# Kernel tuning notes

Hardware: AMD Instinct MI355X
Metric: run time of the kernel (lower is better)

Reference implementation:

```python
import jax, jax.numpy as jnp
import numpy as np

D = 32          # embedding_size
B = 16384       # batch_size
P = 16          # neighbor_sample_size (paths per item per hop)
NE = 100000     # n_entity
NU = 100000     # n_user
NR = 32         # n_relation
N_ITER = 2


def setup_inputs() -> dict:
    key = jax.random.key(0)
    ks = jax.random.split(key, 20)
    s = 0.1
    nrm = lambda k, sh: jax.random.normal(k, sh, dtype=jnp.float32) * s
    inp = {
        "user_table": nrm(ks[0], (NU, D)),
        "ent_table": nrm(ks[1], (NE, D)),
        "rel_table": nrm(ks[2], (NR, D)),
        # PyTorch LSTM params, gate order (i, f, g, o)
        "w_ih0": nrm(ks[3], (4 * D, 2 * D)),
        "w_hh0": nrm(ks[4], (4 * D, D)),
        "b_ih0": nrm(ks[5], (4 * D,)),
        "b_hh0": nrm(ks[6], (4 * D,)),
        "w_ih1": nrm(ks[7], (4 * D, 2 * D)),
        "w_hh1": nrm(ks[8], (4 * D, D)),
        "b_ih1": nrm(ks[9], (4 * D,)),
        "b_hh1": nrm(ks[10], (4 * D,)),
        "agg_w": nrm(ks[11], (D, D)),
        "agg_b": nrm(ks[12], (D,)),
        "users": jax.random.randint(ks[13], (B,), 0, NU),
        "items": jax.random.randint(ks[14], (B,), 0, NE),
        "ratings": jax.random.randint(ks[15], (B,), 0, 2),
        # hop h path table: [n_entity, P, 2*(h+1)+1]; values < 32 valid for both tables
        "lp0": jax.random.randint(ks[16], (NE, P, 3), 0, 32),
        "lp1": jax.random.randint(ks[17], (NE, P, 5), 0, 32),
    }
    return inp


def _lstm_last(seq, w_ih, w_hh, b_ih, b_hh):
    # seq: [N, T, 2D] -> final hidden state [N, D], PyTorch gate order i,f,g,o
    N = seq.shape[0]
    H = w_hh.shape[1]
    bias = b_ih + b_hh

    def step(carry, x):
        h, c = carry
        g = x @ w_ih.T + h @ w_hh.T + bias
        i, f, gg, o = jnp.split(g, 4, axis=-1)
        c = jax.nn.sigmoid(f) * c + jax.nn.sigmoid(i) * jnp.tanh(gg)
        h = jax.nn.sigmoid(o) * jnp.tanh(c)
        return (h, c), None

    h0 = jnp.zeros((N, H), seq.dtype)
    (h, _), _ = jax.lax.scan(step, (h0, h0), jnp.swapaxes(seq, 0, 1))
    return h


def _forward(user_table, ent_table, rel_table, lstm_params, agg_w, agg_b,
             users, items, ratings, lps):
    u = user_table[users]                # [B, D]
    items_emb = ent_table[items]         # [B, D]
    for hop in range(N_ITER):
        lp = lps[hop]
        w_ih, w_hh, b_ih, b_hh = lstm_params[hop]
        il = lp[items]                   # [B, P, 2*(hop+1)+1]
        seed_e = ent_table[il[:, :, 0]]  # [B, P, D]
        u_b = jnp.broadcast_to(u[:, None, :], seed_e.shape)
        first = jnp.concatenate([u_b, seed_e], -1)[:, :, None, :]   # [B,P,1,2D]
        rel_e = rel_table[il[:, :, 1::2]]                            # [B,P,hop+1,D]
        tail_e = ent_table[il[:, :, 2::2]]                           # [B,P,hop+1,D]
        rest = jnp.concatenate([rel_e, tail_e], -1)                  # [B,P,hop+1,2D]
        seq = jnp.concatenate([first, rest], 2).reshape(B * P, hop + 2, 2 * D)
        h = _lstm_last(seq, w_ih, w_hh, b_ih, b_hh)                  # [B*P, D]
        final = h.reshape(B, P, D).sum(axis=1)                       # hidden_out sum
        items_emb = (items_emb + final) @ agg_w.T + agg_b            # 'sum' aggregator
    scores = jnp.sum(u * items_emb, axis=-1)                         # [B]
    r = ratings.astype(scores.dtype)
    # stable BCE on sigmoid(scores)
    loss = -jnp.mean(r * jax.nn.log_sigmoid(scores) + (1.0 - r) * jax.nn.log_sigmoid(-scores))
    return loss, jax.nn.sigmoid(scores)


def reference(user_table, ent_table, rel_table,
              w_ih0, w_hh0, b_ih0, b_hh0,
              w_ih1, w_hh1, b_ih1, b_hh1,
              agg_w, agg_b,
              users, items, ratings, lp0, lp1):
    lstm_params = [(w_ih0, w_hh0, b_ih0, b_hh0), (w_ih1, w_hh1, b_ih1, b_hh1)]
    loss, scores_normalized = _forward(user_table, ent_table, rel_table,
                                       lstm_params, agg_w, agg_b,
                                       users, items, ratings, (lp0, lp1))
    return (loss, scores_normalized, items)
```

## Files before the change

### kernel.cpp

```cpp
#include <hip/hip_runtime.h>
#include <math.h>

#define D  32
#define BN 16384
#define PP 16

typedef __bf16 bf16x8 __attribute__((ext_vector_type(8)));
typedef float  floatx4 __attribute__((ext_vector_type(4)));

#define IMG_BYTES   29184
#define WIH_OFF     0
#define WHH_OFF     18432
#define BIAS_OFF    28672
#define X_OFF       29184
#define H_OFF       38400
#define LDS_BYTES   43520

__device__ __forceinline__ float sigf(float x) {
    float e = __builtin_amdgcn_exp2f(-x * 1.44269504088896341f);
    return __builtin_amdgcn_rcpf(1.0f + e);
}
__device__ __forceinline__ float tanh_fast(float x) {
    float e = __builtin_amdgcn_exp2f(x * 2.88539008177792681f);
    return 1.0f - 2.0f * __builtin_amdgcn_rcpf(e + 1.0f);
}
__device__ __forceinline__ float logsigf(float x) {
    float ax = fabsf(x);
    float l = log1pf(__expf(-ax));
    return (x >= 0.0f) ? -l : x - l;
}

__device__ __forceinline__ void stage16(const float* __restrict__ src, char* dst) {
    const float4* s = (const float4*)src;
    float4 a = s[0], b = s[1], c = s[2], d = s[3];
    bf16x8 lo = { (__bf16)a.x, (__bf16)a.y, (__bf16)a.z, (__bf16)a.w,
                  (__bf16)b.x, (__bf16)b.y, (__bf16)b.z, (__bf16)b.w };
    bf16x8 hi = { (__bf16)c.x, (__bf16)c.y, (__bf16)c.z, (__bf16)c.w,
                  (__bf16)d.x, (__bf16)d.y, (__bf16)d.z, (__bf16)d.w };
    *(bf16x8*)dst        = lo;
    *(bf16x8*)(dst + 16) = hi;
}

__global__ __launch_bounds__(256)
void prep_weights(const float* __restrict__ w_ih, const float* __restrict__ w_hh,
                  const float* __restrict__ b_ih, const float* __restrict__ b_hh,
                  float* __restrict__ img_f)
{
    char* base = (char*)img_f;
    const int t0 = blockIdx.x * 256 + threadIdx.x;
    for (int idx = t0; idx < 8192; idx += 2048) {
        int n = idx >> 6, k = idx & 63;
        ((__bf16*)(base + WIH_OFF))[n * 72 + k] = (__bf16)w_ih[idx];
    }
    for (int idx = t0; idx < 4096; idx += 2048) {
        int n = idx >> 5, k = idx & 31;
        ((__bf16*)(base + WHH_OFF))[n * 40 + k] = (__bf16)w_hh[idx];
    }
    if (t0 < 128)
        ((float*)(base + BIAS_OFF))[t0] = b_ih[t0] + b_hh[t0];
}

template<int L, int T>
__global__ __launch_bounds__(256, 2)
void hop_mfma(const float* __restrict__ user_table,
              const float* __restrict__ ent_table,
              const float* __restrict__ rel_table,
              const float* __restrict__ img,
              const int*   __restrict__ users,
              const int*   __restrict__ items,
              const int*   __restrict__ lp,
              float* __restrict__ final_out)
{
    __shared__ __align__(16) char lds[LDS_BYTES];

    const int tid  = threadIdx.x;
    const int lane = tid & 63;
    const int wave = tid >> 6;

    {
        const float4* g = (const float4*)img;
        float4* l = (float4*)lds;
        #pragma unroll
        for (int i = 0; i < 8; ++i) {
            int idx = i * 256 + tid;
            if (idx < IMG_BYTES / 16) l[idx] = g[idx];
        }
    }
    __syncthreads();

    char* Wih  = lds + WIH_OFF;
    char* Whh  = lds + WHH_OFF;
    const float* bias = (const float*)(lds + BIAS_OFF);
    char* Xl   = lds + X_OFF;
    char* Hl   = lds + H_OFF;

    const int srow  = tid >> 2;
    const int squad = tid & 3;
    const int spair = blockIdx.x * 64 + srow;
    const int sb    = spair >> 4;
    const int sp    = spair & 15;
    const int sitem = items[sb];
    const int suser = users[sb];
    const int* __restrict__ sil = lp + ((size_t)sitem * PP + sp) * L;
    char* sdst = Xl + srow * 144 + squad * 32;

    const int wrow = wave * 16;
    const int am   = wrow + (lane & 15);
    const int ak   = (lane >> 4) * 8;
    const int bnl  = lane & 15;

    float cst[8]  = {0,0,0,0,0,0,0,0};
    float hout[8];
    floatx4 acc[8];
    #pragma unroll
    for (int nt = 0; nt < 8; ++nt) {
        float bv = bias[nt * 16 + bnl];
        floatx4 v = { bv, bv, bv, bv };
        acc[nt] = v;
    }

    #pragma unroll
    for (int t = 0; t < T; ++t) {
        {
            const float* src;
            if (t == 0) {
                src = (squad < 2) ? user_table + (size_t)suser * D + squad * 16
                                  : ent_table + (size_t)sil[0] * D + (squad - 2) * 16;
            } else {
                src = (squad < 2) ? rel_table + (size_t)sil[2 * t - 1] * D + squad * 16
                                  : ent_table + (size_t)sil[2 * t]     * D + (squad - 2) * 16;
            }
            stage16(src, sdst);
        }

        bf16x8 ax0 = *(const bf16x8*)(Xl + am * 144 + ak * 2);
        bf16x8 ax1 = *(const bf16x8*)(Xl + am * 144 + 64 + ak * 2);
        bf16x8 ah  = {};
        if (t > 0) ah = *(const bf16x8*)(Hl + am * 80 + ak * 2);

        #pragma unroll
        for (int nt = 0; nt < 8; ++nt) {
            const int bn = nt * 16 + bnl;
            bf16x8 b0 = *(const bf16x8*)(Wih + bn * 144 + ak * 2);
            bf16x8 b1 = *(const bf16x8*)(Wih + bn * 144 + 64 + ak * 2);
            floatx4 a = acc[nt];
            a = __builtin_amdgcn_mfma_f32_16x16x32_bf16(ax0, b0, a, 0, 0, 0);
            a = __builtin_amdgcn_mfma_f32_16x16x32_bf16(ax1, b1, a, 0, 0, 0);
            if (t > 0) {
                bf16x8 bh = *(const bf16x8*)(Whh + bn * 80 + ak * 2);
                a = __builtin_amdgcn_mfma_f32_16x16x32_bf16(ah, bh, a, 0, 0, 0);
            }
            acc[nt] = a;
        }

        #pragma unroll
        for (int ng = 0; ng < 2; ++ng) {
            floatx4 gi = acc[ng], gf = acc[ng + 2], gg = acc[ng + 4], go = acc[ng + 6];
            #pragma unroll
            for (int r = 0; r < 4; ++r) {
                float c = cst[ng * 4 + r];
                c = sigf(gf[r]) * c + sigf(gi[r]) * tanh_fast(gg[r]);
                cst[ng * 4 + r] = c;
                float h = sigf(go[r]) * tanh_fast(c);
                hout[ng * 4 + r] = h;
                if (t < T - 1) {
                    int pr = wrow + (lane >> 4) * 4 + r;
                    int un = ng * 16 + bnl;
                    *(__bf16*)(Hl + pr * 80 + un * 2) = (__bf16)h;
                }
            }
        }

        if (t < T - 1) {
            #pragma unroll
            for (int nt = 0; nt < 8; ++nt) {
                float bv = bias[nt * 16 + bnl];
                floatx4 v = { bv, bv, bv, bv };
                acc[nt] = v;
            }
        }
    }

    const int fb = blockIdx.x * 4 + wave;
    #pragma unroll
    for (int ng = 0; ng < 2; ++ng) {
        float v = hout[ng * 4 + 0] + hout[ng * 4 + 1] + hout[ng * 4 + 2] + hout[ng * 4 + 3];
        v += __shfl_xor(v, 16);
        v += __shfl_xor(v, 32);
        if (lane < 16)
            final_out[(size_t)fb * D + ng * 16 + lane] = v;
    }
}

__global__ __launch_bounds__(256)
void agg_kernel(const float* __restrict__ src_emb,
                const float* __restrict__ ent_table,
                const int*   __restrict__ items,
                const float* __restrict__ final_in,
                const float* __restrict__ agg_w,
                const float* __restrict__ agg_b,
                float* __restrict__ out_emb)
{
    const int t = blockIdx.x * 256 + threadIdx.x;
    const int b = t >> 5;
    const int j = t & 31;
    const float* __restrict__ src =
        src_emb ? (src_emb + (size_t)b * D) : (ent_table + (size_t)items[b] * D);
    const float* __restrict__ fin = final_in + (size_t)b * D;
    const float* __restrict__ w   = agg_w + (size_t)j * D;
    float acc = agg_b[j];
    #pragma unroll
    for (int k = 0; k < D; ++k) acc = fmaf(src[k] + fin[k], w[k], acc);
    out_emb[t] = acc;
}

__global__ __launch_bounds__(256)
void score_kernel(const float* __restrict__ user_table,
                  const float* __restrict__ emb,
                  const int*   __restrict__ users,
                  const int*   __restrict__ items,
                  const int*   __restrict__ ratings,
                  float* __restrict__ out,
                  float* __restrict__ partials)
{
    __shared__ float red[4];
    const int t = threadIdx.x;
    const int b = blockIdx.x * 256 + t;
    const float* __restrict__ u = user_table + (size_t)users[b] * D;
    const float* __restrict__ e = emb + (size_t)b * D;
    float s = 0.0f;
    #pragma unroll
    for (int k = 0; k < D; ++k) s = fmaf(u[k], e[k], s);
    out[1 + b]      = sigf(s);
    out[1 + BN + b] = (float)items[b];
    float r = (float)ratings[b];
    float term = r * logsigf(s) + (1.0f - r) * logsigf(-s);
    #pragma unroll
    for (int m = 1; m < 64; m <<= 1) term += __shfl_xor(term, m);
    if ((t & 63) == 0) red[t >> 6] = term;
    __syncthreads();
    if (t == 0) partials[blockIdx.x] = red[0] + red[1] + red[2] + red[3];
}

__global__ void loss_kernel(const float* __restrict__ partials, float* __restrict__ out)
{
    const int t = threadIdx.x;
    float v = partials[t];
    #pragma unroll
    for (int m = 1; m < 64; m <<= 1) v += __shfl_xor(v, m);
    if (t == 0) out[0] = -v / (float)BN;
}

extern "C" void kernel_launch(void* const* d_in, const int* in_sizes, int n_in,
                              void* d_out, int out_size, void* d_ws, size_t ws_size,
                              hipStream_t stream)
{
    const float* user_table = (const float*)d_in[0];
    const float* ent_table  = (const float*)d_in[1];
    const float* rel_table  = (const float*)d_in[2];
    const float* w_ih0 = (const float*)d_in[3];
    const float* w_hh0 = (const float*)d_in[4];
    const float* b_ih0 = (const float*)d_in[5];
    const float* b_hh0 = (const float*)d_in[6];
    const float* w_ih1 = (const float*)d_in[7];
    const float* w_hh1 = (const float*)d_in[8];
    const float* b_ih1 = (const float*)d_in[9];
    const float* b_hh1 = (const float*)d_in[10];
    const float* agg_w = (const float*)d_in[11];
    const float* agg_b = (const float*)d_in[12];
    const int* users   = (const int*)d_in[13];
    const int* items   = (const int*)d_in[14];
    const int* ratings = (const int*)d_in[15];
    const int* lp0     = (const int*)d_in[16];
    const int* lp1     = (const int*)d_in[17];
    float* out = (float*)d_out;

    float* ws        = (float*)d_ws;
    float* final_buf = ws;
    float* emb0      = ws + (size_t)BN * D;
    float* emb1      = ws + 2 * (size_t)BN * D;
    float* partials  = ws + 3 * (size_t)BN * D;
    float* img0      = ws + 3 * (size_t)BN * D + 64;
    float* img1      = img0 + IMG_BYTES / 4;

    prep_weights<<<8, 256, 0, stream>>>(w_ih0, w_hh0, b_ih0, b_hh0, img0);
    prep_weights<<<8, 256, 0, stream>>>(w_ih1, w_hh1, b_ih1, b_hh1, img1);

    const int hop_blocks = (BN * PP) / 64;
    hop_mfma<3, 2><<<hop_blocks, 256, 0, stream>>>(
        user_table, ent_table, rel_table, img0, users, items, lp0, final_buf);
    agg_kernel<<<(BN * D) / 256, 256, 0, stream>>>(
        nullptr, ent_table, items, final_buf, agg_w, agg_b, emb0);
    hop_mfma<5, 3><<<hop_blocks, 256, 0, stream>>>(
        user_table, ent_table, rel_table, img1, users, items, lp1, final_buf);
    agg_kernel<<<(BN * D) / 256, 256, 0, stream>>>(
        emb0, ent_table, items, final_buf, agg_w, agg_b, emb1);
    score_kernel<<<BN / 256, 256, 0, stream>>>(
        user_table, emb1, users, items, ratings, out, partials);
    loss_kernel<<<1, 64, 0, stream>>>(partials, out);
}
```

Baseline: 249.3 us.

## Fuse aggregator into hop kernel and keep LSTM weights in registers

The separate aggregation kernel is folded into the end of each hop kernel. Each wave writes its summed hidden state plus the source embedding into LDS, then applies the agg linear layer from an LDS copy of agg_w. This removes the final_buf round trip and two kernel launches. LSTM weight fragments and bias are also loaded once into registers instead of being re-read from LDS every timestep, and the LDS layout is reused for X/H. The cost is higher register pressure, which may lower occupancy under launch_bounds(256,2).

```diff
diff --git a/kernel.cpp b/kernel.cpp
--- a/kernel.cpp
+++ b/kernel.cpp
@@ -8,13 +8,15 @@
 typedef __bf16 bf16x8 __attribute__((ext_vector_type(8)));
 typedef float  floatx4 __attribute__((ext_vector_type(4)));
 
-#define IMG_BYTES   29184
 #define WIH_OFF     0
 #define WHH_OFF     18432
 #define BIAS_OFF    28672
-#define X_OFF       29184
-#define H_OFF       38400
-#define LDS_BYTES   43520
+#define AGG_OFF     29184
+#define AGGB_OFF    33792
+#define IMG_BYTES   33920
+#define X_OFF       0
+#define H_OFF       9216
+#define S_OFF       14336
 
 __device__ __forceinline__ float sigf(float x) {
     float e = __builtin_amdgcn_exp2f(-x * 1.44269504088896341f);
@@ -44,6 +46,7 @@
 __global__ __launch_bounds__(256)
 void prep_weights(const float* __restrict__ w_ih, const float* __restrict__ w_hh,
                   const float* __restrict__ b_ih, const float* __restrict__ b_hh,
+                  const float* __restrict__ agg_w, const float* __restrict__ agg_b,
                   float* __restrict__ img_f)
 {
     char* base = (char*)img_f;
@@ -58,6 +61,12 @@
     }
     if (t0 < 128)
         ((float*)(base + BIAS_OFF))[t0] = b_ih[t0] + b_hh[t0];
+    if (t0 < 1024) {
+        int r = t0 >> 5, k = t0 & 31;
+        ((float*)(base + AGG_OFF))[r * 36 + k] = agg_w[t0];
+    }
+    if (t0 < 32)
+        ((float*)(base + AGGB_OFF))[t0] = agg_b[t0];
 }
 
 template<int L, int T>
@@ -69,9 +78,10 @@
               const int*   __restrict__ users,
               const int*   __restrict__ items,
               const int*   __restrict__ lp,
-              float* __restrict__ final_out)
-{
-    __shared__ __align__(16) char lds[LDS_BYTES];
+              const float* __restrict__ src_emb,
+              float* __restrict__ emb_out)
+{
+    __shared__ __align__(16) char lds[IMG_BYTES];
 
     const int tid  = threadIdx.x;
     const int lane = tid & 63;
@@ -81,41 +91,53 @@
         const float4* g = (const float4*)img;
         float4* l = (float4*)lds;
         #pragma unroll
-        for (int i = 0; i < 8; ++i) {
+        for (int i = 0; i < 9; ++i) {
             int idx = i * 256 + tid;
             if (idx < IMG_BYTES / 16) l[idx] = g[idx];
         }
     }
     __syncthreads();
 
-    char* Wih  = lds + WIH_OFF;
-    char* Whh  = lds + WHH_OFF;
-    const float* bias = (const float*)(lds + BIAS_OFF);
-    char* Xl   = lds + X_OFF;
-    char* Hl   = lds + H_OFF;
+    const int ak  = (lane >> 4) * 8;
+    const int bnl = lane & 15;
+
+    bf16x8 wb0[8], wb1[8], wbh[8];
+    float  biasv[8];
+    {
+        const char* Wih = lds + WIH_OFF;
+        const char* Whh = lds + WHH_OFF;
+        const float* bias = (const float*)(lds + BIAS_OFF);
+        #pragma unroll
+        for (int nt = 0; nt < 8; ++nt) {
+            const int bn = nt * 16 + bnl;
+            wb0[nt] = *(const bf16x8*)(Wih + bn * 144 + ak * 2);
+            wb1[nt] = *(const bf16x8*)(Wih + bn * 144 + 64 + ak * 2);
+            wbh[nt] = *(const bf16x8*)(Whh + bn * 80 + ak * 2);
+            biasv[nt] = bias[nt * 16 + bnl];
+        }
+    }
+    __syncthreads();
+
+    char* Xl = lds + X_OFF;
+    char* Hl = lds + H_OFF;
 
     const int srow  = tid >> 2;
     const int squad = tid & 3;
     const int spair = blockIdx.x * 64 + srow;
     const int sb    = spair >> 4;
-    const int sp    = spair & 15;
-    const int sitem = items[sb];
+    const int* __restrict__ sil = lp + ((size_t)items[sb] * PP + (spair & 15)) * L;
     const int suser = users[sb];
-    const int* __restrict__ sil = lp + ((size_t)sitem * PP + sp) * L;
     char* sdst = Xl + srow * 144 + squad * 32;
 
     const int wrow = wave * 16;
     const int am   = wrow + (lane & 15);
-    const int ak   = (lane >> 4) * 8;
-    const int bnl  = lane & 15;
 
     float cst[8]  = {0,0,0,0,0,0,0,0};
     float hout[8];
     floatx4 acc[8];
     #pragma unroll
     for (int nt = 0; nt < 8; ++nt) {
-        float bv = bias[nt * 16 + bnl];
-        floatx4 v = { bv, bv, bv, bv };
+        floatx4 v = { biasv[nt], biasv[nt], biasv[nt], biasv[nt] };
         acc[nt] = v;
     }
 
@@ -140,16 +162,11 @@
 
         #pragma unroll
         for (int nt = 0; nt < 8; ++nt) {
-            const int bn = nt * 16 + bnl;
-            bf16x8 b0 = *(const bf16x8*)(Wih + bn * 144 + ak * 2);
-            bf16x8 b1 = *(const bf16x8*)(Wih + bn * 144 + 64 + ak * 2);
             floatx4 a = acc[nt];
-            a = __builtin_amdgcn_mfma_f32_16x16x32_bf16(ax0, b0, a, 0, 0, 0);
-            a = __builtin_amdgcn_mfma_f32_16x16x32_bf16(ax1, b1, a, 0, 0, 0);
-            if (t > 0) {
-                bf16x8 bh = *(const bf16x8*)(Whh + bn * 80 + ak * 2);
-                a = __builtin_amdgcn_mfma_f32_16x16x32_bf16(ah, bh, a, 0, 0, 0);
-            }
+            a = __builtin_amdgcn_mfma_f32_16x16x32_bf16(ax0, wb0[nt], a, 0, 0, 0);
+            a = __builtin_amdgcn_mfma_f32_16x16x32_bf16(ax1, wb1[nt], a, 0, 0, 0);
+            if (t > 0)
+                a = __builtin_amdgcn_mfma_f32_16x16x32_bf16(ah, wbh[nt], a, 0, 0, 0);
             acc[nt] = a;
         }
 
@@ -165,8 +182,7 @@
                 hout[ng * 4 + r] = h;
                 if (t < T - 1) {
                     int pr = wrow + (lane >> 4) * 4 + r;
-                    int un = ng * 16 + bnl;
-                    *(__bf16*)(Hl + pr * 80 + un * 2) = (__bf16)h;
+                    *(__bf16*)(Hl + pr * 80 + (ng * 16 + bnl) * 2) = (__bf16)h;
                 }
             }
         }
@@ -174,44 +190,34 @@
         if (t < T - 1) {
             #pragma unroll
             for (int nt = 0; nt < 8; ++nt) {
-                float bv = bias[nt * 16 + bnl];
-                floatx4 v = { bv, bv, bv, bv };
+                floatx4 v = { biasv[nt], biasv[nt], biasv[nt], biasv[nt] };
                 acc[nt] = v;
             }
         }
     }
 
     const int fb = blockIdx.x * 4 + wave;
+    float* s_l = (float*)(lds + S_OFF + wave * 128);
     #pragma unroll
     for (int ng = 0; ng < 2; ++ng) {
         float v = hout[ng * 4 + 0] + hout[ng * 4 + 1] + hout[ng * 4 + 2] + hout[ng * 4 + 3];
         v += __shfl_xor(v, 16);
         v += __shfl_xor(v, 32);
-        if (lane < 16)
-            final_out[(size_t)fb * D + ng * 16 + lane] = v;
-    }
-}
-
-__global__ __launch_bounds__(256)
-void agg_kernel(const float* __restrict__ src_emb,
-                const float* __restrict__ ent_table,
-                const int*   __restrict__ items,
-                const float* __restrict__ final_in,
-                const float* __restrict__ agg_w,
-                const float* __restrict__ agg_b,
-                float* __restrict__ out_emb)
-{
-    const int t = blockIdx.x * 256 + threadIdx.x;
-    const int b = t >> 5;
-    const int j = t & 31;
-    const float* __restrict__ src =
-        src_emb ? (src_emb + (size_t)b * D) : (ent_table + (size_t)items[b] * D);
-    const float* __restrict__ fin = final_in + (size_t)b * D;
-    const float* __restrict__ w   = agg_w + (size_t)j * D;
-    float acc = agg_b[j];
-    #pragma unroll
-    for (int k = 0; k < D; ++k) acc = fmaf(src[k] + fin[k], w[k], acc);
-    out_emb[t] = acc;
+        if (lane < 16) {
+            const int k = ng * 16 + lane;
+            float s = src_emb ? src_emb[(size_t)fb * D + k]
+                              : ent_table[(size_t)items[fb] * D + k];
+            s_l[k] = s + v;
+        }
+    }
+    __syncthreads();
+    if (lane < 32) {
+        const float* aw = (const float*)(lds + AGG_OFF) + lane * 36;
+        float acc_o = ((const float*)(lds + AGGB_OFF))[lane];
+        #pragma unroll
+        for (int k = 0; k < D; ++k) acc_o = fmaf(s_l[k], aw[k], acc_o);
+        emb_out[(size_t)fb * D + lane] = acc_o;
+    }
 }
 
 __global__ __launch_bounds__(256)
@@ -275,26 +281,21 @@
     const int* lp1     = (const int*)d_in[17];
     float* out = (float*)d_out;
 
-    float* ws        = (float*)d_ws;
-    float* final_buf = ws;
-    float* emb0      = ws + (size_t)BN * D;
-    float* emb1      = ws + 2 * (size_t)BN * D;
-    float* partials  = ws + 3 * (size_t)BN * D;
-    float* img0      = ws + 3 * (size_t)BN * D + 64;
-    float* img1      = img0 + IMG_BYTES / 4;
-
-    prep_weights<<<8, 256, 0, stream>>>(w_ih0, w_hh0, b_ih0, b_hh0, img0);
-    prep_weights<<<8, 256, 0, stream>>>(w_ih1, w_hh1, b_ih1, b_hh1, img1);
+    float* ws       = (float*)d_ws;
+    float* emb0     = ws;
+    float* emb1     = ws + (size_t)BN * D;
+    float* partials = ws + 2 * (size_t)BN * D;
+    float* img0     = ws + 2 * (size_t)BN * D + 64;
+    float* img1     = img0 + IMG_BYTES / 4;
+
+    prep_weights<<<8, 256, 0, stream>>>(w_ih0, w_hh0, b_ih0, b_hh0, agg_w, agg_b, img0);
+    prep_weights<<<8, 256, 0, stream>>>(w_ih1, w_hh1, b_ih1, b_hh1, agg_w, agg_b, img1);
 
     const int hop_blocks = (BN * PP) / 64;
     hop_mfma<3, 2><<<hop_blocks, 256, 0, stream>>>(
-        user_table, ent_table, rel_table, img0, users, items, lp0, final_buf);
-    agg_kernel<<<(BN * D) / 256, 256, 0, stream>>>(
-        nullptr, ent_table, items, final_buf, agg_w, agg_b, emb0);
+        user_table, ent_table, rel_table, img0, users, items, lp0, nullptr, emb0);
     hop_mfma<5, 3><<<hop_blocks, 256, 0, stream>>>(
-        user_table, ent_table, rel_table, img1, users, items, lp1, final_buf);
-    agg_kernel<<<(BN * D) / 256, 256, 0, stream>>>(
-        emb0, ent_table, items, final_buf, agg_w, agg_b, emb1);
+        user_table, ent_table, rel_table, img1, users, items, lp1, emb0, emb1);
     score_kernel<<<BN / 256, 256, 0, stream>>>(
         user_table, emb1, users, items, ratings, out, partials);
     loss_kernel<<<1, 64, 0, stream>>>(partials, out);
```

Result: no change. 249.7 us (+0.2%).
